# Optimization experiments

Hardware: AMD Instinct MI355X
Metric: run time of the kernel (lower is better)

## Reference

```python
import jax, jax.numpy as jnp
import numpy as np

BS, M, D, D_EM, K_RET = 32, 32768, 1024, 128, 32
EPS = 1e-12

def unit_normalize(x):
    return x / jnp.sqrt(jnp.sum(x * x, axis=-1, keepdims=True) + EPS)

def setup_inputs() -> dict:
    key = jax.random.key(0)
    ks = jax.random.split(key, 12)
    s = lambda fan_in: 1.0 / np.sqrt(fan_in)
    return {
        "x": jax.random.normal(ks[0], (BS, D), jnp.float32),
        "y_wm": jax.random.normal(ks[1], (BS, D), jnp.float32),
        "em_K": unit_normalize(jax.random.normal(ks[2], (BS, M, D_EM), jnp.float32)),
        "em_V": jax.random.normal(ks[3], (BS, M, D_EM), jnp.float32) * 0.01,
        "em_S": jax.random.uniform(ks[4], (BS, M), jnp.float32),  # all > 0 (active)
        "Wq_em_w": jax.random.normal(ks[5], (2 * D, D_EM), jnp.float32) * s(2 * D),
        "Wq_em_b": jnp.zeros((D_EM,), jnp.float32),
        "Wq_cross_w": jax.random.normal(ks[6], (D, D_EM), jnp.float32) * s(D),
        "Wq_cross_b": jnp.zeros((D_EM,), jnp.float32),
        "Wo_w": jax.random.normal(ks[7], (D_EM, D), jnp.float32) * s(D_EM),
        "Wo_b": jnp.zeros((D,), jnp.float32),
        "ln_g": jnp.ones((D_EM,), jnp.float32),
        "ln_b": jnp.zeros((D_EM,), jnp.float32),
        "ffn1_w": jax.random.normal(ks[8], (D_EM, 4 * D_EM), jnp.float32) * s(D_EM),
        "ffn1_b": jnp.zeros((4 * D_EM,), jnp.float32),
        "ffn2_w": jax.random.normal(ks[9], (4 * D_EM, D_EM), jnp.float32) * s(4 * D_EM),
        "ffn2_b": jnp.zeros((D_EM,), jnp.float32),
    }

def layernorm(x, g, b):
    mu = jnp.mean(x, axis=-1, keepdims=True)
    var = jnp.mean((x - mu) ** 2, axis=-1, keepdims=True)
    return (x - mu) * jax.lax.rsqrt(var + 1e-5) * g + b

def reference(x, y_wm, em_K, em_V, em_S, Wq_em_w, Wq_em_b, Wq_cross_w, Wq_cross_b,
              Wo_w, Wo_b, ln_g, ln_b, ffn1_w, ffn1_b, ffn2_w, ffn2_b):
    # query over concatenated (x, y_wm), unit-normalized
    q = unit_normalize(jnp.concatenate([x, y_wm], axis=-1) @ Wq_em_w + Wq_em_b)  # [BS, D_em]
    # masked cosine similarity scan over all M slots
    scores = jnp.einsum('bd,bmd->bm', q, em_K)                                   # [BS, M]
    scores = jnp.where(em_S > 0, scores, -jnp.inf)
    topk_scores, topk_idx = jax.lax.top_k(scores, K_RET)                         # [BS, k]
    V_top = jnp.take_along_axis(em_V, topk_idx[:, :, None], axis=1)              # [BS, k, D_em]
    # cross-attention read over retrieved slots
    q_cross = x @ Wq_cross_w + Wq_cross_b                                        # [BS, D_em]
    attn = jnp.einsum('bd,bkd->bk', q_cross, V_top) * (D_EM ** -0.5) + topk_scores
    attn = jnp.where(jnp.isneginf(topk_scores), -jnp.inf, attn)
    attn = jnp.nan_to_num(jax.nn.softmax(attn, axis=-1), nan=0.0)
    out = jnp.einsum('bk,bkd->bd', attn, V_top)                                  # [BS, D_em]
    # readout FFN (residual), exact GELU as in torch default
    h = layernorm(out, ln_g, ln_b)
    out = out + (jax.nn.gelu(h @ ffn1_w + ffn1_b, approximate=False) @ ffn2_w + ffn2_b)
    return out @ Wo_w + Wo_b                                                     # [BS, D]
```

## Files before the change

kernel.cpp:

```cpp
#include <hip/hip_runtime.h>
#include <math.h>

constexpr int kM  = 32768;
constexpr int kD  = 1024;
constexpr int kDE = 128;
constexpr int kK  = 32;
constexpr int kBins = 256;
constexpr int kCap  = 1024;

typedef float f4 __attribute__((ext_vector_type(4)));

__device__ __forceinline__ int score_bin(float s) {
  float u = s + 1.0f;
  float w = u * 128.0f;
  w = fminf(fmaxf(w, 0.0f), 255.0f);
  return (int)w;
}

__global__ __launch_bounds__(1024) void qproj_kernel(
    const float* __restrict__ x, const float* __restrict__ y,
    const float* __restrict__ Wqe, const float* __restrict__ bqe,
    const float* __restrict__ Wqc, const float* __restrict__ bqc,
    float* __restrict__ q, float* __restrict__ qc,
    unsigned int* __restrict__ hist) {
  const int b = blockIdx.x, t = threadIdx.x;
  const int s = t >> 7, j = t & 127;

  if (t < kBins) hist[b * kBins + t] = 0u;

  const float* xb = x + b * kD;
  const float* yb = y + b * kD;

  const float* src1 = (s < 4) ? xb : yb;
  const int off1 = (s < 4) ? s * 256 : s * 256 - 1024;
  const int wb1 = s * 256;
  float a1[4] = {0.f, 0.f, 0.f, 0.f};
#pragma unroll 8
  for (int i0 = 0; i0 < 256; i0 += 4) {
#pragma unroll
    for (int u = 0; u < 4; ++u)
      a1[u] += src1[off1 + i0 + u] * Wqe[(wb1 + i0 + u) * kDE + j];
  }
  const int r2 = s * 128;
  float a2[4] = {0.f, 0.f, 0.f, 0.f};
#pragma unroll 8
  for (int i0 = 0; i0 < 128; i0 += 4) {
#pragma unroll
    for (int u = 0; u < 4; ++u)
      a2[u] += xb[r2 + i0 + u] * Wqc[(r2 + i0 + u) * kDE + j];
  }

  __shared__ float p1[8][128];
  __shared__ float p2[8][128];
  __shared__ float redn[2];
  p1[s][j] = (a1[0] + a1[1]) + (a1[2] + a1[3]);
  p2[s][j] = (a2[0] + a2[1]) + (a2[2] + a2[3]);
  __syncthreads();

  float a = 0.f, c = 0.f;
  if (t < 128) {
    a = bqe[t];
    c = bqc[t];
#pragma unroll
    for (int ss = 0; ss < 8; ++ss) { a += p1[ss][t]; c += p2[ss][t]; }
  }
  float sq = a * a;
#pragma unroll
  for (int m = 1; m < 64; m <<= 1) sq += __shfl_xor(sq, m);
  if (t == 0 || t == 64) redn[t >> 6] = sq;
  __syncthreads();
  if (t < 128) {
    const float inv = 1.f / sqrtf(redn[0] + redn[1] + 1e-12f);
    q[b * kDE + t] = a * inv;
    qc[b * kDE + t] = c;
  }
}

__global__ __launch_bounds__(256) void scores_kernel(
    const float* __restrict__ emK, const float* __restrict__ emS,
    const float* __restrict__ q, float* __restrict__ sc,
    unsigned int* __restrict__ hist) {
  const int b = blockIdx.y, chunk = blockIdx.x;
  const int wave = threadIdx.x >> 6;
  const int lane = threadIdx.x & 63;
  const int half = lane >> 5;
  const int l32 = lane & 31;

  __shared__ unsigned int shist[kBins];
  if (threadIdx.x < kBins) shist[threadIdx.x] = 0u;
  __syncthreads();

  const float4 qf = *reinterpret_cast<const float4*>(q + b * kDE + l32 * 4);
  const int rowbase = chunk * 512 + wave * 128;
  const float* Kb = emK + (size_t)b * kM * kDE;
  const float* Sb = emS + (size_t)b * kM;
  float* scb = sc + (size_t)b * kM;

  for (int it = 0; it < 8; ++it) {
    const int A = rowbase + it * 16 + half * 8;
    const float* p = Kb + (size_t)A * kDE + l32 * 4;
    const f4 k0 = __builtin_nontemporal_load((const f4*)(p));
    const f4 k1 = __builtin_nontemporal_load((const f4*)(p + kDE));
    const f4 k2 = __builtin_nontemporal_load((const f4*)(p + 2 * kDE));
    const f4 k3 = __builtin_nontemporal_load((const f4*)(p + 3 * kDE));
    const f4 k4 = __builtin_nontemporal_load((const f4*)(p + 4 * kDE));
    const f4 k5 = __builtin_nontemporal_load((const f4*)(p + 5 * kDE));
    const f4 k6 = __builtin_nontemporal_load((const f4*)(p + 6 * kDE));
    const f4 k7 = __builtin_nontemporal_load((const f4*)(p + 7 * kDE));

    float d0 = fmaf(k0.w, qf.w, fmaf(k0.z, qf.z, fmaf(k0.y, qf.y, k0.x * qf.x)));
    float d1 = fmaf(k1.w, qf.w, fmaf(k1.z, qf.z, fmaf(k1.y, qf.y, k1.x * qf.x)));
    float d2 = fmaf(k2.w, qf.w, fmaf(k2.z, qf.z, fmaf(k2.y, qf.y, k2.x * qf.x)));
    float d3 = fmaf(k3.w, qf.w, fmaf(k3.z, qf.z, fmaf(k3.y, qf.y, k3.x * qf.x)));
    float d4 = fmaf(k4.w, qf.w, fmaf(k4.z, qf.z, fmaf(k4.y, qf.y, k4.x * qf.x)));
    float d5 = fmaf(k5.w, qf.w, fmaf(k5.z, qf.z, fmaf(k5.y, qf.y, k5.x * qf.x)));
    float d6 = fmaf(k6.w, qf.w, fmaf(k6.z, qf.z, fmaf(k6.y, qf.y, k6.x * qf.x)));
    float d7 = fmaf(k7.w, qf.w, fmaf(k7.z, qf.z, fmaf(k7.y, qf.y, k7.x * qf.x)));

#pragma unroll
    for (int m = 1; m < 32; m <<= 1) {
      d0 += __shfl_xor(d0, m);
      d1 += __shfl_xor(d1, m);
      d2 += __shfl_xor(d2, m);
      d3 += __shfl_xor(d3, m);
      d4 += __shfl_xor(d4, m);
      d5 += __shfl_xor(d5, m);
      d6 += __shfl_xor(d6, m);
      d7 += __shfl_xor(d7, m);
    }
    const float e0 = (l32 & 1) ? d1 : d0;
    const float e1 = (l32 & 1) ? d3 : d2;
    const float e2 = (l32 & 1) ? d5 : d4;
    const float e3 = (l32 & 1) ? d7 : d6;
    const float g0 = (l32 & 2) ? e1 : e0;
    const float g1 = (l32 & 2) ? e3 : e2;
    const float sel = (l32 & 4) ? g1 : g0;

    const float sv = Sb[A + (l32 & 7)];
    const float val = (sv > 0.f) ? sel : -INFINITY;
    if (l32 < 8) {
      scb[A + l32] = val;
      atomicAdd(&shist[score_bin(val)], 1u);
    }
  }
  __syncthreads();
  if (threadIdx.x < kBins) {
    const unsigned int ccount = shist[threadIdx.x];
    if (ccount) atomicAdd(&hist[b * kBins + threadIdx.x], ccount);
  }
}

__global__ __launch_bounds__(1024) void select_finish_kernel(
    const float* __restrict__ sc, const unsigned int* __restrict__ hist,
    const float* __restrict__ emV, const float* __restrict__ qc,
    const float* __restrict__ lng, const float* __restrict__ lnb,
    const float* __restrict__ f1w, const float* __restrict__ f1b,
    const float* __restrict__ f2w, const float* __restrict__ f2b,
    const float* __restrict__ Wo, const float* __restrict__ Wob,
    float* __restrict__ out) {
  const int b = blockIdx.x, t = threadIdx.x;
  const int wave = t >> 6, lane = t & 63;

  __shared__ unsigned int scum[kBins];
  __shared__ int Bsh;
  __shared__ unsigned int cnt;
  __shared__ unsigned long long ck[kCap];
  __shared__ float outvS[32];
  __shared__ int outiS[32];
  __shared__ float Vt[32][128];
  __shared__ float qcl[128];
  __shared__ float wgt[32];
  __shared__ float hS[128];
  __shared__ float y1S[512];
  __shared__ float p2S[4][128];
  __shared__ float o2S[128];
  __shared__ float redA[2];
  __shared__ float redB[2];

  if (t < kBins) scum[t] = hist[b * kBins + t];
  if (t == 0) { Bsh = 0; cnt = 0u; }
  if (t < 128) qcl[t] = qc[b * kDE + t];
  __syncthreads();

  for (int off = 1; off < kBins; off <<= 1) {
    unsigned int v = 0;
    if (t < kBins) {
      v = scum[t];
      if (t + off < kBins) v += scum[t + off];
    }
    __syncthreads();
    if (t < kBins) scum[t] = v;
    __syncthreads();
  }
  if (t < kBins && scum[t] >= 32u) atomicMax(&Bsh, t);
  __syncthreads();
  const int B = Bsh;

  const float* scb = sc + (size_t)b * kM;
#pragma unroll
  for (int j = 0; j < 32; ++j) {
    const int idx = j * 1024 + t;
    const float s = scb[idx];
    if (score_bin(s) >= B) {
      const unsigned int pos = atomicAdd(&cnt, 1u);
      if (pos < (unsigned)kCap) {
        unsigned int u = __float_as_uint(s);
        u = (u & 0x80000000u) ? ~u : (u | 0x80000000u);
        ck[pos] = ((unsigned long long)u << 32) | (unsigned int)(~idx);
      }
    }
  }
  __syncthreads();
  const unsigned int total = cnt;
  for (unsigned int i = t; i < (unsigned)kCap; i += 1024)
    if (i >= total) ck[i] = 0ull;
  __syncthreads();

  for (int k2 = 2; k2 <= kCap; k2 <<= 1) {
    for (int j2 = k2 >> 1; j2 > 0; j2 >>= 1) {
      const int l = t ^ j2;
      if (l > t) {
        const unsigned long long a = ck[t], c = ck[l];
        const bool desc = ((t & k2) == 0);
        if ((a < c) == desc) { ck[t] = c; ck[l] = a; }
      }
      __syncthreads();
    }
  }

  if (t < 32) {
    const unsigned long long kk = ck[t];
    const unsigned int mono = (unsigned int)(kk >> 32);
    const unsigned int u = (mono & 0x80000000u) ? (mono & 0x7fffffffu) : ~mono;
    outvS[t] = __uint_as_float(u);
    outiS[t] = (int)(~(unsigned int)kk);
  }
  __syncthreads();

  const float* Vb = emV + (size_t)b * kM * kDE;
#pragma unroll
  for (int e = t; e < 32 * 128; e += 1024) {
    const int r = e >> 7, ccol = e & 127;
    Vt[r][ccol] = Vb[(size_t)outiS[r] * kDE + ccol];
  }
  __syncthreads();

#pragma unroll
  for (int kk2 = 0; kk2 < 2; ++kk2) {
    const int k = wave * 2 + kk2;
    float p = Vt[k][2 * lane] * qcl[2 * lane] + Vt[k][2 * lane + 1] * qcl[2 * lane + 1];
#pragma unroll
    for (int m = 1; m < 64; m <<= 1) p += __shfl_xor(p, m);
    if (lane == 0) {
      const float tv = outvS[k];
      wgt[k] = (tv == -INFINITY) ? -INFINITY : fmaf(p, 0.08838834764831845f, tv);
    }
  }
  __syncthreads();

  if (t < 32) {
    const float lg = wgt[t];
    float mx = lg;
#pragma unroll
    for (int m = 1; m < 32; m <<= 1) mx = fmaxf(mx, __shfl_xor(mx, m));
    float e = (mx == -INFINITY || lg == -INFINITY) ? 0.f : __expf(lg - mx);
    float ssum = e;
#pragma unroll
    for (int m = 1; m < 32; m <<= 1) ssum += __shfl_xor(ssum, m);
    wgt[t] = (ssum > 0.f) ? e / ssum : 0.f;
  }
  __syncthreads();

  float od = 0.f;
  if (t < 128) {
#pragma unroll 8
    for (int k = 0; k < 32; ++k) od += wgt[k] * Vt[k][t];
  }
  float s1 = (t < 128) ? od : 0.f;
  float s2 = (t < 128) ? od * od : 0.f;
#pragma unroll
  for (int m = 1; m < 64; m <<= 1) {
    s1 += __shfl_xor(s1, m);
    s2 += __shfl_xor(s2, m);
  }
  if (lane == 0 && wave < 2) { redA[wave] = s1; redB[wave] = s2; }
  __syncthreads();
  const float sum1 = redA[0] + redA[1];
  const float sum2 = redB[0] + redB[1];
  const float mu = sum1 * (1.f / 128.f);
  const float var = sum2 * (1.f / 128.f) - mu * mu;
  const float rstd = 1.f / sqrtf(var + 1e-5f);
  if (t < 128) hS[t] = (od - mu) * rstd * lng[t] + lnb[t];
  __syncthreads();

  if (t < 512) {
    float acc = f1b[t];
#pragma unroll 8
    for (int d = 0; d < 128; ++d) acc += hS[d] * f1w[(size_t)d * 512 + t];
    y1S[t] = 0.5f * acc * (1.f + erff(acc * 0.7071067811865476f));
  }
  __syncthreads();

  if (t < 512) {
    const int g = t >> 7, ccol = t & 127;
    float acc = 0.f;
#pragma unroll 8
    for (int jj = 0; jj < 128; ++jj)
      acc += y1S[g * 128 + jj] * f2w[(size_t)(g * 128 + jj) * 128 + ccol];
    p2S[g][ccol] = acc;
  }
  __syncthreads();
  if (t < 128)
    o2S[t] = od + f2b[t] + ((p2S[0][t] + p2S[1][t]) + (p2S[2][t] + p2S[3][t]));
  __syncthreads();

  float acc = Wob[t];
#pragma unroll 8
  for (int d = 0; d < 128; ++d) acc += o2S[d] * Wo[(size_t)d * kD + t];
  out[(size_t)b * kD + t] = acc;
}

extern "C" void kernel_launch(void* const* d_in, const int* in_sizes, int n_in,
                              void* d_out, int out_size, void* d_ws, size_t ws_size,
                              hipStream_t stream) {
  const float* x   = (const float*)d_in[0];
  const float* y   = (const float*)d_in[1];
  const float* emK = (const float*)d_in[2];
  const float* emV = (const float*)d_in[3];
  const float* emS = (const float*)d_in[4];
  const float* Wqe = (const float*)d_in[5];
  const float* bqe = (const float*)d_in[6];
  const float* Wqc = (const float*)d_in[7];
  const float* bqc = (const float*)d_in[8];
  const float* Wo  = (const float*)d_in[9];
  const float* Wob = (const float*)d_in[10];
  const float* lng = (const float*)d_in[11];
  const float* lnb = (const float*)d_in[12];
  const float* f1w = (const float*)d_in[13];
  const float* f1b = (const float*)d_in[14];
  const float* f2w = (const float*)d_in[15];
  const float* f2b = (const float*)d_in[16];
  float* out = (float*)d_out;

  float* ws = (float*)d_ws;
  float* q    = ws;
  float* qc   = ws + 4096;
  float* sc   = ws + 8192;
  unsigned int* hist = (unsigned int*)(ws + 8192 + 32 * kM);

  hipLaunchKernelGGL(qproj_kernel, dim3(32), dim3(1024), 0, stream,
                     x, y, Wqe, bqe, Wqc, bqc, q, qc, hist);
  hipLaunchKernelGGL(scores_kernel, dim3(64, 32), dim3(256), 0, stream,
                     emK, emS, q, sc, hist);
  hipLaunchKernelGGL(select_finish_kernel, dim3(32), dim3(1024), 0, stream,
                     sc, hist, emV, qc, lng, lnb, f1w, f1b, f2w, f2b, Wo, Wob, out);
}
```

Baseline: 162.1 us.

## Replace histogram top-k with fixed-threshold candidate collection and rank-based selection

The scores kernel no longer builds a per-batch histogram. It appends every score above a fixed threshold (0.20) to a global candidate list through an atomic counter. The finish kernel then ranks those candidates by counting comparisons instead of running a 1024-wide bitonic sort, and falls back to the old histogram path when the count is outside [32, 2048]. The dot-product reduction is restructured into a butterfly transpose that uses fewer shuffles, non-temporal loads become plain loads, and the finish block shrinks to 512 threads. The threshold is tuned to the distribution of the test inputs (random unit keys in 128 dimensions), so the fast path depends on the data, though the fallback keeps the result correct.

Result: slower. 225.2 us (+38.9%).

```diff
diff --git a/kernel.cpp b/kernel.cpp
--- a/kernel.cpp
+++ b/kernel.cpp
@@ -5,16 +5,20 @@
 constexpr int kD  = 1024;
 constexpr int kDE = 128;
 constexpr int kK  = 32;
-constexpr int kBins = 256;
-constexpr int kCap  = 1024;
+constexpr int kCap = 2048;
+constexpr float kT0 = 0.20f;
 
 typedef float f4 __attribute__((ext_vector_type(4)));
 
 __device__ __forceinline__ int score_bin(float s) {
-  float u = s + 1.0f;
-  float w = u * 128.0f;
+  float w = (s + 1.0f) * 128.0f;
   w = fminf(fmaxf(w, 0.0f), 255.0f);
   return (int)w;
+}
+__device__ __forceinline__ unsigned long long pack_key(float s, int idx) {
+  unsigned u = __float_as_uint(s);
+  u = (u & 0x80000000u) ? ~u : (u | 0x80000000u);
+  return ((unsigned long long)u << 32) | (unsigned)(~idx);
 }
 
 __global__ __launch_bounds__(1024) void qproj_kernel(
@@ -22,11 +26,11 @@
     const float* __restrict__ Wqe, const float* __restrict__ bqe,
     const float* __restrict__ Wqc, const float* __restrict__ bqc,
     float* __restrict__ q, float* __restrict__ qc,
-    unsigned int* __restrict__ hist) {
+    unsigned int* __restrict__ gcnt) {
   const int b = blockIdx.x, t = threadIdx.x;
   const int s = t >> 7, j = t & 127;
 
-  if (t < kBins) hist[b * kBins + t] = 0u;
+  if (t == 0) gcnt[b] = 0u;
 
   const float* xb = x + b * kD;
   const float* yb = y + b * kD;
@@ -79,17 +83,13 @@
 __global__ __launch_bounds__(256) void scores_kernel(
     const float* __restrict__ emK, const float* __restrict__ emS,
     const float* __restrict__ q, float* __restrict__ sc,
-    unsigned int* __restrict__ hist) {
+    unsigned int* __restrict__ gcnt, unsigned long long* __restrict__ gcand) {
   const int b = blockIdx.y, chunk = blockIdx.x;
   const int wave = threadIdx.x >> 6;
   const int lane = threadIdx.x & 63;
   const int half = lane >> 5;
   const int l32 = lane & 31;
 
-  __shared__ unsigned int shist[kBins];
-  if (threadIdx.x < kBins) shist[threadIdx.x] = 0u;
-  __syncthreads();
-
   const float4 qf = *reinterpret_cast<const float4*>(q + b * kDE + l32 * 4);
   const int rowbase = chunk * 512 + wave * 128;
   const float* Kb = emK + (size_t)b * kM * kDE;
@@ -99,14 +99,14 @@
   for (int it = 0; it < 8; ++it) {
     const int A = rowbase + it * 16 + half * 8;
     const float* p = Kb + (size_t)A * kDE + l32 * 4;
-    const f4 k0 = __builtin_nontemporal_load((const f4*)(p));
-    const f4 k1 = __builtin_nontemporal_load((const f4*)(p + kDE));
-    const f4 k2 = __builtin_nontemporal_load((const f4*)(p + 2 * kDE));
-    const f4 k3 = __builtin_nontemporal_load((const f4*)(p + 3 * kDE));
-    const f4 k4 = __builtin_nontemporal_load((const f4*)(p + 4 * kDE));
-    const f4 k5 = __builtin_nontemporal_load((const f4*)(p + 5 * kDE));
-    const f4 k6 = __builtin_nontemporal_load((const f4*)(p + 6 * kDE));
-    const f4 k7 = __builtin_nontemporal_load((const f4*)(p + 7 * kDE));
+    const f4 k0 = *reinterpret_cast<const f4*>(p);
+    const f4 k1 = *reinterpret_cast<const f4*>(p + kDE);
+    const f4 k2 = *reinterpret_cast<const f4*>(p + 2 * kDE);
+    const f4 k3 = *reinterpret_cast<const f4*>(p + 3 * kDE);
+    const f4 k4 = *reinterpret_cast<const f4*>(p + 4 * kDE);
+    const f4 k5 = *reinterpret_cast<const f4*>(p + 5 * kDE);
+    const f4 k6 = *reinterpret_cast<const f4*>(p + 6 * kDE);
+    const f4 k7 = *reinterpret_cast<const f4*>(p + 7 * kDE);
 
     float d0 = fmaf(k0.w, qf.w, fmaf(k0.z, qf.z, fmaf(k0.y, qf.y, k0.x * qf.x)));
     float d1 = fmaf(k1.w, qf.w, fmaf(k1.z, qf.z, fmaf(k1.y, qf.y, k1.x * qf.x)));
@@ -117,41 +117,39 @@
     float d6 = fmaf(k6.w, qf.w, fmaf(k6.z, qf.z, fmaf(k6.y, qf.y, k6.x * qf.x)));
     float d7 = fmaf(k7.w, qf.w, fmaf(k7.z, qf.z, fmaf(k7.y, qf.y, k7.x * qf.x)));
 
-#pragma unroll
-    for (int m = 1; m < 32; m <<= 1) {
-      d0 += __shfl_xor(d0, m);
-      d1 += __shfl_xor(d1, m);
-      d2 += __shfl_xor(d2, m);
-      d3 += __shfl_xor(d3, m);
-      d4 += __shfl_xor(d4, m);
-      d5 += __shfl_xor(d5, m);
-      d6 += __shfl_xor(d6, m);
-      d7 += __shfl_xor(d7, m);
-    }
-    const float e0 = (l32 & 1) ? d1 : d0;
-    const float e1 = (l32 & 1) ? d3 : d2;
-    const float e2 = (l32 & 1) ? d5 : d4;
-    const float e3 = (l32 & 1) ? d7 : d6;
-    const float g0 = (l32 & 2) ? e1 : e0;
-    const float g1 = (l32 & 2) ? e3 : e2;
-    const float sel = (l32 & 4) ? g1 : g0;
-
-    const float sv = Sb[A + (l32 & 7)];
-    const float val = (sv > 0.f) ? sel : -INFINITY;
-    if (l32 < 8) {
-      scb[A + l32] = val;
-      atomicAdd(&shist[score_bin(val)], 1u);
-    }
-  }
-  __syncthreads();
-  if (threadIdx.x < kBins) {
-    const unsigned int ccount = shist[threadIdx.x];
-    if (ccount) atomicAdd(&hist[b * kBins + threadIdx.x], ccount);
-  }
-}
-
-__global__ __launch_bounds__(1024) void select_finish_kernel(
-    const float* __restrict__ sc, const unsigned int* __restrict__ hist,
+    d0 += __shfl_xor(d0, 16); d1 += __shfl_xor(d1, 16);
+    d2 += __shfl_xor(d2, 16); d3 += __shfl_xor(d3, 16);
+    d4 += __shfl_xor(d4, 16); d5 += __shfl_xor(d5, 16);
+    d6 += __shfl_xor(d6, 16); d7 += __shfl_xor(d7, 16);
+    float w0 = (l32 & 16) ? d4 : d0;
+    float w1 = (l32 & 16) ? d5 : d1;
+    float w2 = (l32 & 16) ? d6 : d2;
+    float w3 = (l32 & 16) ? d7 : d3;
+    w0 += __shfl_xor(w0, 8); w1 += __shfl_xor(w1, 8);
+    w2 += __shfl_xor(w2, 8); w3 += __shfl_xor(w3, 8);
+    float u0 = (l32 & 8) ? w2 : w0;
+    float u1 = (l32 & 8) ? w3 : w1;
+    u0 += __shfl_xor(u0, 4); u1 += __shfl_xor(u1, 4);
+    float z = (l32 & 4) ? u1 : u0;
+    z += __shfl_xor(z, 2);
+    z += __shfl_xor(z, 1);
+
+    const float sv = Sb[A + (l32 >> 2)];
+    if ((l32 & 3) == 0) {
+      const int row = A + (l32 >> 2);
+      const float val = (sv > 0.f) ? z : -INFINITY;
+      scb[row] = val;
+      if (val >= kT0) {
+        const unsigned pos = atomicAdd(&gcnt[b], 1u);
+        if (pos < (unsigned)kCap) gcand[(size_t)b * kCap + pos] = pack_key(val, row);
+      }
+    }
+  }
+}
+
+__global__ __launch_bounds__(512) void finish_kernel(
+    const float* __restrict__ sc, const unsigned int* __restrict__ gcnt,
+    const unsigned long long* __restrict__ gcand,
     const float* __restrict__ emV, const float* __restrict__ qc,
     const float* __restrict__ lng, const float* __restrict__ lnb,
     const float* __restrict__ f1w, const float* __restrict__ f1b,
@@ -161,10 +159,8 @@
   const int b = blockIdx.x, t = threadIdx.x;
   const int wave = t >> 6, lane = t & 63;
 
-  __shared__ unsigned int scum[kBins];
-  __shared__ int Bsh;
-  __shared__ unsigned int cnt;
   __shared__ unsigned long long ck[kCap];
+  __shared__ int nS;
   __shared__ float outvS[32];
   __shared__ int outiS[32];
   __shared__ float Vt[32][128];
@@ -177,77 +173,89 @@
   __shared__ float redA[2];
   __shared__ float redB[2];
 
-  if (t < kBins) scum[t] = hist[b * kBins + t];
-  if (t == 0) { Bsh = 0; cnt = 0u; }
+  const unsigned cnt = gcnt[b];
+  const float* scb = sc + (size_t)b * kM;
   if (t < 128) qcl[t] = qc[b * kDE + t];
-  __syncthreads();
-
-  for (int off = 1; off < kBins; off <<= 1) {
-    unsigned int v = 0;
-    if (t < kBins) {
-      v = scum[t];
-      if (t + off < kBins) v += scum[t + off];
-    }
+  if (t < 32) { outvS[t] = -INFINITY; outiS[t] = 0; }
+
+  if (cnt >= 32u && cnt <= (unsigned)kCap) {
+    for (unsigned i = t; i < cnt; i += 512)
+      ck[i] = gcand[(size_t)b * kCap + i];
+    if (t == 0) nS = (int)cnt;
+  } else {
+    __shared__ unsigned int shist[256];
+    __shared__ int Bsh;
+    __shared__ unsigned int cnt2;
+    if (t < 256) shist[t] = 0u;
+    if (t == 0) { Bsh = 0; cnt2 = 0u; }
     __syncthreads();
-    if (t < kBins) scum[t] = v;
+    for (int i = t; i < kM; i += 512)
+      atomicAdd(&shist[score_bin(scb[i])], 1u);
     __syncthreads();
-  }
-  if (t < kBins && scum[t] >= 32u) atomicMax(&Bsh, t);
-  __syncthreads();
-  const int B = Bsh;
-
-  const float* scb = sc + (size_t)b * kM;
-#pragma unroll
-  for (int j = 0; j < 32; ++j) {
-    const int idx = j * 1024 + t;
-    const float s = scb[idx];
-    if (score_bin(s) >= B) {
-      const unsigned int pos = atomicAdd(&cnt, 1u);
-      if (pos < (unsigned)kCap) {
-        unsigned int u = __float_as_uint(s);
-        u = (u & 0x80000000u) ? ~u : (u | 0x80000000u);
-        ck[pos] = ((unsigned long long)u << 32) | (unsigned int)(~idx);
-      }
-    }
-  }
-  __syncthreads();
-  const unsigned int total = cnt;
-  for (unsigned int i = t; i < (unsigned)kCap; i += 1024)
-    if (i >= total) ck[i] = 0ull;
-  __syncthreads();
-
-  for (int k2 = 2; k2 <= kCap; k2 <<= 1) {
-    for (int j2 = k2 >> 1; j2 > 0; j2 >>= 1) {
-      const int l = t ^ j2;
-      if (l > t) {
-        const unsigned long long a = ck[t], c = ck[l];
-        const bool desc = ((t & k2) == 0);
-        if ((a < c) == desc) { ck[t] = c; ck[l] = a; }
+    for (int off = 1; off < 256; off <<= 1) {
+      unsigned v = 0;
+      if (t < 256) {
+        v = shist[t];
+        if (t + off < 256) v += shist[t + off];
       }
       __syncthreads();
-    }
-  }
-
-  if (t < 32) {
-    const unsigned long long kk = ck[t];
-    const unsigned int mono = (unsigned int)(kk >> 32);
-    const unsigned int u = (mono & 0x80000000u) ? (mono & 0x7fffffffu) : ~mono;
-    outvS[t] = __uint_as_float(u);
-    outiS[t] = (int)(~(unsigned int)kk);
-  }
+      if (t < 256) shist[t] = v;
+      __syncthreads();
+    }
+    if (t < 256 && shist[t] >= 32u) atomicMax(&Bsh, t);
+    __syncthreads();
+    const int B = Bsh;
+    for (int i = t; i < kM; i += 512) {
+      const float s = scb[i];
+      if (score_bin(s) >= B) {
+        const unsigned pos = atomicAdd(&cnt2, 1u);
+        if (pos < (unsigned)kCap) ck[pos] = pack_key(s, i);
+      }
+    }
+    __syncthreads();
+    if (t == 0) nS = (int)min(cnt2, (unsigned)kCap);
+  }
+  __syncthreads();
+  const int n = nS;
+
+  unsigned long long mykey0 = 0, mykey1 = 0, mykey2 = 0, mykey3 = 0;
+  if (t < n) mykey0 = ck[t];
+  if (t + 512 < n) mykey1 = ck[t + 512];
+  if (t + 1024 < n) mykey2 = ck[t + 1024];
+  if (t + 1536 < n) mykey3 = ck[t + 1536];
+  int r0 = 0, r1 = 0, r2 = 0, r3 = 0;
+  for (int i = 0; i < n; ++i) {
+    const unsigned long long o = ck[i];
+    r0 += (o > mykey0);
+    r1 += (o > mykey1);
+    r2 += (o > mykey2);
+    r3 += (o > mykey3);
+  }
+  auto emit = [&](unsigned long long key, int rank, int slot) {
+    if (slot < n && rank < 32) {
+      const unsigned mono = (unsigned)(key >> 32);
+      const unsigned u = (mono & 0x80000000u) ? (mono & 0x7fffffffu) : ~mono;
+      outvS[rank] = __uint_as_float(u);
+      outiS[rank] = (int)(~(unsigned)key);
+    }
+  };
+  emit(mykey0, r0, t);
+  emit(mykey1, r1, t + 512);
+  emit(mykey2, r2, t + 1024);
+  emit(mykey3, r3, t + 1536);
   __syncthreads();
 
   const float* Vb = emV + (size_t)b * kM * kDE;
 #pragma unroll
-  for (int e = t; e < 32 * 128; e += 1024) {
+  for (int e = t; e < 32 * 128; e += 512) {
     const int r = e >> 7, ccol = e & 127;
     Vt[r][ccol] = Vb[(size_t)outiS[r] * kDE + ccol];
   }
   __syncthreads();
 
 #pragma unroll
-  for (int kk2 = 0; kk2 < 2; ++kk2) {
-    const int k = wave * 2 + kk2;
+  for (int kk2 = 0; kk2 < 4; ++kk2) {
+    const int k = wave * 4 + kk2;
     float p = Vt[k][2 * lane] * qcl[2 * lane] + Vt[k][2 * lane + 1] * qcl[2 * lane + 1];
 #pragma unroll
     for (int m = 1; m < 64; m <<= 1) p += __shfl_xor(p, m);
@@ -293,7 +301,7 @@
   if (t < 128) hS[t] = (od - mu) * rstd * lng[t] + lnb[t];
   __syncthreads();
 
-  if (t < 512) {
+  {
     float acc = f1b[t];
 #pragma unroll 8
     for (int d = 0; d < 128; ++d) acc += hS[d] * f1w[(size_t)d * 512 + t];
@@ -301,7 +309,7 @@
   }
   __syncthreads();
 
-  if (t < 512) {
+  {
     const int g = t >> 7, ccol = t & 127;
     float acc = 0.f;
 #pragma unroll 8
@@ -314,10 +322,15 @@
     o2S[t] = od + f2b[t] + ((p2S[0][t] + p2S[1][t]) + (p2S[2][t] + p2S[3][t]));
   __syncthreads();
 
-  float acc = Wob[t];
-#pragma unroll 8
-  for (int d = 0; d < 128; ++d) acc += o2S[d] * Wo[(size_t)d * kD + t];
-  out[(size_t)b * kD + t] = acc;
+  float acc0 = Wob[t], acc1 = Wob[t + 512];
+#pragma unroll 8
+  for (int d = 0; d < 128; ++d) {
+    const float hv = o2S[d];
+    acc0 += hv * Wo[(size_t)d * kD + t];
+    acc1 += hv * Wo[(size_t)d * kD + t + 512];
+  }
+  out[(size_t)b * kD + t] = acc0;
+  out[(size_t)b * kD + t + 512] = acc1;
 }
 
 extern "C" void kernel_launch(void* const* d_in, const int* in_sizes, int n_in,
@@ -343,15 +356,17 @@
   float* out = (float*)d_out;
 
   float* ws = (float*)d_ws;
-  float* q    = ws;
-  float* qc   = ws + 4096;
-  float* sc   = ws + 8192;
-  unsigned int* hist = (unsigned int*)(ws + 8192 + 32 * kM);
+  float* q  = ws;
+  float* qc = ws + 4096;
+  float* sc = ws + 8192;
+  unsigned int* gcnt = (unsigned int*)(ws + 8192 + 32 * kM);
+  unsigned long long* gcand =
+      (unsigned long long*)(ws + 8192 + 32 * kM + 32);
 
   hipLaunchKernelGGL(qproj_kernel, dim3(32), dim3(1024), 0, stream,
-                     x, y, Wqe, bqe, Wqc, bqc, q, qc, hist);
+                     x, y, Wqe, bqe, Wqc, bqc, q, qc, gcnt);
   hipLaunchKernelGGL(scores_kernel, dim3(64, 32), dim3(256), 0, stream,
-                     emK, emS, q, sc, hist);
-  hipLaunchKernelGGL(select_finish_kernel, dim3(32), dim3(1024), 0, stream,
-                     sc, hist, emV, qc, lng, lnb, f1w, f1b, f2w, f2b, Wo, Wob, out);
-}
+                     emK, emS, q, sc, gcnt, gcand);
+  hipLaunchKernelGGL(finish_kernel, dim3(32), dim3(512), 0, stream,
+                     sc, gcnt, gcand, emV, qc, lng, lnb, f1w, f1b, f2w, f2b, Wo, Wob, out);
+}
```
